# Performance work log

Measured on AMD Instinct MI355X. Metric: run time of the kernel, lower is better.

## Reference

```python
import jax, jax.numpy as jnp
import numpy as np

VOLRADIUS = 256.0
DT = 1.0 / VOLRADIUS  # self.dt = dt / volradius with dt=1.0
N_STEPS = 64
B, H, W, K, M = 1, 256, 256, 64, 16


def setup_inputs() -> dict:
    rng = np.random.default_rng(0)
    # orthographic-ish ray bundle looking down +z through the primitive cloud
    ys, xs = np.meshgrid(np.linspace(-1., 1., H, dtype=np.float32),
                         np.linspace(-1., 1., W, dtype=np.float32), indexing='ij')
    raypos = np.broadcast_to(np.stack([xs, ys, np.full_like(xs, -0.125)], -1)[None],
                             (B, H, W, 3)).astype(np.float32).copy()
    raydir = np.zeros((B, H, W, 3), np.float32); raydir[..., 2] = 1.0
    tmin = np.zeros((B, H, W), np.float32)
    tminmax = np.stack([tmin, tmin + N_STEPS * DT], -1).astype(np.float32)
    # primpos is in WORLD units (module divides by volradius)
    primpos = rng.uniform(-0.1 * VOLRADIUS, 0.1 * VOLRADIUS, (B, K, 3)).astype(np.float32)
    q, _ = np.linalg.qr(rng.normal(size=(B, K, 3, 3)))
    primrot = q.astype(np.float32)
    primscale = rng.uniform(8., 16., (B, K, 3)).astype(np.float32)  # inverse half-extent
    primrgba = rng.uniform(0., 1., (B, K, 4, M, M, M)).astype(np.float32)
    return {
        'raypos': jnp.asarray(raypos), 'raydir': jnp.asarray(raydir),
        'tminmax': jnp.asarray(tminmax), 'primpos': jnp.asarray(primpos),
        'primrot': jnp.asarray(primrot), 'primscale': jnproundtrip(primscale) if False else jnp.asarray(primscale),
        'primrgba': jnp.asarray(primrgba),
    }


def _trilinear_sum(template, pos, primpos, primrot, primscale):
    # template [K,4,M,M,M]; pos [R,3]; returns summed rgba over primitives [R,4]
    Mv = template.shape[-1]
    kidx = jnp.arange(template.shape[0])[None, :]                      # [1,K]
    rel = pos[:, None, :] - primpos[None, :, :]                        # [R,K,3]
    # local = primscale * (primrot^T @ rel), inside prim iff |local| < 1
    local = jnp.einsum('kij,rki->rkj', primrot, rel) * primscale[None]  # [R,K,3]
    inside = jnp.all(jnp.abs(local) < 1.0, axis=-1)                    # [R,K]
    g = jnp.clip((local + 1.0) * 0.5 * (Mv - 1), 0.0, Mv - 1 - 1e-5)    # voxel coords (x,y,z)
    i0 = jnp.clip(jnp.floor(g).astype(jnp.int32), 0, Mv - 2)
    f = g - i0.astype(g.dtype)
    x0, y0, z0 = i0[..., 0], i0[..., 1], i0[..., 2]
    fx, fy, fz = f[..., 0], f[..., 1], f[..., 2]
    c = jnp.zeros(local.shape[:2] + (4,), template.dtype)
    for dz, wz in ((0, 1 - fz), (1, fz)):
        for dy, wy in ((0, 1 - fy), (1, fy)):
            for dx, wx in ((0, 1 - fx), (1, fx)):
                corner = template[kidx, :, z0 + dz, y0 + dy, x0 + dx]  # [R,K,4]
                c = c + corner * (wz * wy * wx)[..., None]
    c = c * inside[..., None]
    return c.sum(axis=1)                                               # [R,4]


def _march(raypos, raydir, tminmax, primpos, primrot, primscale, template):
    Hh, Ww, _ = raypos.shape
    R = Hh * Ww
    o = raypos.reshape(R, 3)
    d = raydir.reshape(R, 3)
    tmm = tminmax.reshape(R, 2)
    tmin, tmax = tmm[:, 0], tmm[:, 1]

    def step(carry, i):
        rgb, alpha = carry
        t = tmin + (i.astype(jnp.float32) + 0.5) * DT
        valid = t < tmax
        pos = o + t[:, None] * d
        s = _trilinear_sum(template, pos, primpos, primrot, primscale)  # [R,4]
        # MVP front-to-back saturating alpha compositing (early-term equivalent)
        contrib = jnp.minimum(1.0, alpha + s[:, 3] * DT) - alpha
        contrib = jnp.where(valid, contrib, 0.0)
        rgb = rgb + s[:, :3] * contrib[:, None]
        alpha = alpha + contrib
        return (rgb, alpha), None

    init = (jnp.zeros((R, 3), jnp.float32), jnp.zeros((R,), jnp.float32))
    (rgb, alpha), _ = jax.lax.scan(jax.checkpoint(step), init, jnp.arange(N_STEPS))
    return jnp.concatenate([rgb, alpha[:, None]], -1).reshape(Hh, Ww, 4)


def reference(raypos, raydir, tminmax, primpos, primrot, primscale, primrgba):
    primpos_n = primpos / VOLRADIUS  # module normalizes primpos by volume radius
    rayrgba = jax.vmap(_march)(raypos, raydir, tminmax, primpos_n, primrot, primscale, primrgba)
    rayrgba = jnp.transpose(rayrgba, (0, 3, 1, 2))  # [B,4,H,W]
    rayrgb = rayrgba[:, :3]
    rayalpha = rayrgba[:, 3:4]
    return rayrgb, rayalpha, rayrgba
```

## Files before the change

kernel.cpp:

```cpp
#include <hip/hip_runtime.h>
#include <hip/hip_fp16.h>

#define Rtot 65536
#define Wimg 256
#define Kp 64
#define NSTEPS 64
#define DTc (1.0f/256.0f)
#define INV_VOLR (1.0f/256.0f)
#define NITEMS 16384
#define HOTGRID 2048

#define PD_OFF    0u
#define TB_OFF    4096u
#define FLAG_OFF  20480u
#define QC_OFF    36864u
#define QUEUE_OFF 40960u
#define LIST_OFF  131072u
#define TT_OFF    2097152u
#define SBUF_OFF  8388608u
#define WS_NEED   (SBUF_OFF + (size_t)NITEMS*256*8)

typedef _Float16 half2v __attribute__((ext_vector_type(2)));

__device__ __forceinline__ half2v u2h(unsigned int u) {
  union { unsigned int u; half2v h; } x; x.u = u; return x.h;
}
__device__ __forceinline__ half2v mkh2(float a, float b) {
  half2v h; h.x = (_Float16)a; h.y = (_Float16)b; return h;
}
__device__ __forceinline__ unsigned int pack2(float a, float b) {
  __half2 h = __floats2half2_rn(a, b);
  return *(unsigned int*)&h;
}

#if __has_builtin(__builtin_amdgcn_fdot2)
#define FDOT2(a, b, c) __builtin_amdgcn_fdot2((a), (b), (c), false)
#else
#define FDOT2(a, b, c) ((float)(a).x*(float)(b).x + (float)(a).y*(float)(b).y + (c))
#endif

__global__ __launch_bounds__(256) void setup_kernel(
    const float* __restrict__ raypos, const float* __restrict__ raydir,
    const float* __restrict__ tminmax, const float* __restrict__ primpos,
    const float* __restrict__ primrot, const float* __restrict__ primscale,
    const float* __restrict__ tmpl,
    float* __restrict__ tb, unsigned long long* __restrict__ tth,
    float* __restrict__ pd, int* __restrict__ qc) {
  int bid = blockIdx.x, tid = threadIdx.x;
  if (bid < 256) {
    __shared__ float smn[4][7], smx[4][7];
    int w = (bid & 15)*16 + (tid & 15);
    int h = (bid >> 4)*16 + (tid >> 4);
    int r = h*Wimg + w;
    float v[7];
    v[0] = raypos[r*3+0]; v[1] = raypos[r*3+1]; v[2] = raypos[r*3+2];
    v[3] = raydir[r*3+0]; v[4] = raydir[r*3+1]; v[5] = raydir[r*3+2];
    v[6] = tminmax[r*2+0];
    float mn[7], mx[7];
#pragma unroll
    for (int i = 0; i < 7; ++i) { mn[i] = v[i]; mx[i] = v[i]; }
#pragma unroll
    for (int m = 1; m < 64; m <<= 1) {
#pragma unroll
      for (int i = 0; i < 7; ++i) {
        mn[i] = fminf(mn[i], __shfl_xor(mn[i], m));
        mx[i] = fmaxf(mx[i], __shfl_xor(mx[i], m));
      }
    }
    int wv = tid >> 6;
    if ((tid & 63) == 0) {
#pragma unroll
      for (int i = 0; i < 7; ++i) { smn[wv][i] = mn[i]; smx[wv][i] = mx[i]; }
    }
    __syncthreads();
    if (tid == 0) {
#pragma unroll
      for (int i = 0; i < 7; ++i) {
        tb[bid*16 + i]     = fminf(fminf(smn[0][i], smn[1][i]), fminf(smn[2][i], smn[3][i]));
        tb[bid*16 + 8 + i] = fmaxf(fmaxf(smx[0][i], smx[1][i]), fmaxf(smx[2][i], smx[3][i]));
      }
    }
  } else if (bid < 512) {
    int k = (bid - 256) >> 2;
    int q = (bid - 256) & 3;
    const float* b0 = tmpl + (((size_t)k) << 14);
    unsigned long long* o = tth + (k << 12);
#pragma unroll
    for (int s = 0; s < 4; ++s) {
      int v = q*1024 + s*256 + tid;
      unsigned long long lo = pack2(b0[v],      b0[4096+v]);
      unsigned long long hi = pack2(b0[8192+v], b0[12288+v]);
      o[v] = lo | (hi << 32);
    }
  } else {
    int k = tid;
    if (k == Kp) qc[0] = 0;
    if (k < Kp) {
      float sc0 = primscale[k*3+0], sc1 = primscale[k*3+1], sc2 = primscale[k*3+2];
      float* o = pd + (k << 4);
      o[0] = primpos[k*3+0] * INV_VOLR;
      o[1] = primpos[k*3+1] * INV_VOLR;
      o[2] = primpos[k*3+2] * INV_VOLR;
      o[3] = 0.0f; o[4] = 0.0f; o[5] = 0.0f;
#pragma unroll
      for (int i = 0; i < 3; ++i) {
        o[6+i*3+0] = primrot[k*9+i*3+0]*sc0;
        o[6+i*3+1] = primrot[k*9+i*3+1]*sc1;
        o[6+i*3+2] = primrot[k*9+i*3+2]*sc2;
      }
      o[15] = 0.0f;
    }
  }
}

__global__ __launch_bounds__(256) void cull_kernel(
    const float* __restrict__ pd, const float* __restrict__ tb,
    unsigned char* __restrict__ flags, unsigned char* __restrict__ lists,
    int* __restrict__ queue, int* __restrict__ qc) {
  int wv = threadIdx.x >> 6, lane = threadIdx.x & 63;
  int item = blockIdx.x*4 + wv;
  int tile = item >> 6, step = item & 63;
  const float* t0 = tb + tile*16;
  float cst = ((float)step + 0.5f)*DTc;
  float tl = t0[6] + cst, th = t0[14] + cst;
  const float* p = pd + (lane << 4);
  float rlo[3], rhi[3];
#pragma unroll
  for (int a = 0; a < 3; ++a) {
    float ol = t0[a], oh = t0[8+a], dl = t0[3+a], dh = t0[11+a];
    float p1 = tl*dl, p2 = tl*dh, p3 = th*dl, p4 = th*dh;
    rlo[a] = ol + fminf(fminf(p1, p2), fminf(p3, p4)) - p[a];
    rhi[a] = oh + fmaxf(fmaxf(p1, p2), fmaxf(p3, p4)) - p[a];
  }
  bool pass = true;
#pragma unroll
  for (int j = 0; j < 3; ++j) {
    float llo = 0.f, lhi = 0.f;
#pragma unroll
    for (int a = 0; a < 3; ++a) {
      float rsc = p[6+a*3+j];
      float q1 = rlo[a]*rsc, q2 = rhi[a]*rsc;
      llo += fminf(q1, q2);
      lhi += fmaxf(q1, q2);
    }
    pass = pass && (llo < 1.0f) && (lhi > -1.0f);
  }
  unsigned long long mask = __ballot(pass);
  int cnt = (int)__popcll(mask);
  if (lane == 0) flags[item] = (unsigned char)(cnt > 0 ? 1 : 0);
  if (pass) {
    int pos = (int)__popcll(mask & ((1ull << lane) - 1ull));
    lists[item*64 + pos] = (unsigned char)lane;
  }
  if (cnt > 0 && lane == 0) {
    int qpos = atomicAdd(qc, 1);
    queue[qpos] = item | (cnt << 16);
  }
}

#define ACC_CORNER(va, vb, wc) {                                             \
    unsigned int alo = (unsigned int)(va), ahi = (unsigned int)((va) >> 32); \
    unsigned int blo = (unsigned int)(vb), bhi = (unsigned int)((vb) >> 32); \
    half2v wp = mkh2((wc)*wx0, (wc)*fx);                                     \
    unsigned int p0 = (alo & 0xFFFFu) | (blo << 16);                         \
    unsigned int p1 = (alo >> 16)     | (bhi ? (blo & 0xFFFF0000u) : (blo & 0xFFFF0000u)); \
    unsigned int p2 = (ahi & 0xFFFFu) | (bhi << 16);                         \
    unsigned int p3 = (ahi >> 16)     | (bhi & 0xFFFF0000u);                 \
    c0 = FDOT2(u2h(p0), wp, c0);                                             \
    c1 = FDOT2(u2h(p1), wp, c1);                                             \
    c2 = FDOT2(u2h(p2), wp, c2);                                             \
    c3 = FDOT2(u2h(p3), wp, c3); }

__global__ __launch_bounds__(256) void shade_kernel(
    const float* __restrict__ raypos, const float* __restrict__ raydir,
    const float* __restrict__ tminmax, const float* __restrict__ pd,
    const unsigned long long* __restrict__ tv,
    const unsigned char* __restrict__ lists,
    const int* __restrict__ queue, const int* __restrict__ qc,
    unsigned long long* __restrict__ sbuf) {
  __shared__ int s_list[Kp];
  int qn = qc[0];
  int tid = threadIdx.x;
  for (int it = blockIdx.x; it < qn; it += HOTGRID) {
    int entry = queue[it];
    int item = entry & 0xFFFF;
    int cnt0 = entry >> 16;
    int tile = item >> 6, step = item & 63;
    __syncthreads();
    if (tid < cnt0) s_list[tid] = lists[item*64 + tid];
    __syncthreads();
    int w = (tile & 15)*16 + (tid & 15);
    int h = (tile >> 4)*16 + (tid >> 4);
    int r = h*Wimg + w;
    float t = tminmax[r*2] + ((float)step + 0.5f)*DTc;
    float px = fmaf(t, raydir[r*3+0], raypos[r*3+0]);
    float py = fmaf(t, raydir[r*3+1], raypos[r*3+1]);
    float pz = fmaf(t, raydir[r*3+2], raypos[r*3+2]);
    float c0 = 0.f, c1 = 0.f, c2 = 0.f, c3 = 0.f;

    for (int j = 0; j < cnt0; ++j) {
      int k = __builtin_amdgcn_readfirstlane(s_list[j]);
      const float* p = pd + (k << 4);
      float relx = px - p[0], rely = py - p[1], relz = pz - p[2];
      float lx = relx*p[6] + rely*p[9]  + relz*p[12];
      float ly = relx*p[7] + rely*p[10] + relz*p[13];
      float lz = relx*p[8] + rely*p[11] + relz*p[14];
      bool inside = fabsf(lx) < 1.0f && fabsf(ly) < 1.0f && fabsf(lz) < 1.0f;
      if (!__any(inside)) continue;
      if (inside) {
        float gx = fminf(fmaxf((lx + 1.0f)*7.5f, 0.0f), 14.99999f);
        float gy = fminf(fmaxf((ly + 1.0f)*7.5f, 0.0f), 14.99999f);
        float gz = fminf(fmaxf((lz + 1.0f)*7.5f, 0.0f), 14.99999f);
        int ix = (int)gx, iy = (int)gy, iz = (int)gz;
        float fx = gx - (float)ix, fy = gy - (float)iy, fz = gz - (float)iz;
        int idx = (k << 12) + iz*256 + iy*16 + ix;
        unsigned long long v00 = tv[idx],       v01 = tv[idx + 1];
        unsigned long long v10 = tv[idx + 16],  v11 = tv[idx + 17];
        unsigned long long v20 = tv[idx + 256], v21 = tv[idx + 257];
        unsigned long long v30 = tv[idx + 272], v31 = tv[idx + 273];
        float wx0 = 1.0f - fx;
        float wy0 = 1.0f - fy, wz0 = 1.0f - fz;
        float w00 = wz0*wy0, w01 = wz0*fy, w10 = fz*wy0, w11 = fz*fy;
        ACC_CORNER(v00, v01, w00)
        ACC_CORNER(v10, v11, w01)
        ACC_CORNER(v20, v21, w10)
        ACC_CORNER(v30, v31, w11)
      }
    }
    unsigned long long pk = ((unsigned long long)pack2(c2, c3) << 32)
                          | (unsigned long long)pack2(c0, c1);
    sbuf[item*256 + tid] = pk;
  }
}

__global__ __launch_bounds__(256) void composite_kernel(
    const float* __restrict__ tminmax, const unsigned long long* __restrict__ sbuf,
    const unsigned char* __restrict__ flags, float* __restrict__ out) {
  __shared__ unsigned char s_flags[NSTEPS];
  int tid = threadIdx.x;
  int b = blockIdx.x;
  if (tid < NSTEPS) s_flags[tid] = flags[b*NSTEPS + tid];
  __syncthreads();
  int w = (b & 15)*16 + (tid & 15);
  int h = (b >> 4)*16 + (tid >> 4);
  int r = h*Wimg + w;
  float tmin = tminmax[r*2+0], tmax = tminmax[r*2+1];
  float rgb0 = 0.f, rgb1 = 0.f, rgb2 = 0.f, alpha = 0.f;
  for (int i = 0; i < NSTEPS; ++i) {
    float s0 = 0.f, s1 = 0.f, s2 = 0.f, s3 = 0.f;
    if (s_flags[i]) {
      unsigned long long pk = sbuf[(b*NSTEPS + i)*256 + tid];
      unsigned int lo = (unsigned int)pk, hi = (unsigned int)(pk >> 32);
      float2 lf = __half22float2(*(__half2*)&lo);
      float2 hf = __half22float2(*(__half2*)&hi);
      s0 = lf.x; s1 = lf.y; s2 = hf.x; s3 = hf.y;
    }
    float t = tmin + ((float)i + 0.5f)*DTc;
    float contrib = fminf(1.0f, fmaf(s3, DTc, alpha)) - alpha;
    contrib = (t < tmax) ? contrib : 0.0f;
    rgb0 = fmaf(s0, contrib, rgb0);
    rgb1 = fmaf(s1, contrib, rgb1);
    rgb2 = fmaf(s2, contrib, rgb2);
    alpha += contrib;
  }
  out[0*Rtot + r] = rgb0;
  out[1*Rtot + r] = rgb1;
  out[2*Rtot + r] = rgb2;
  out[3*Rtot + r] = alpha;
  out[4*Rtot + r] = rgb0;
  out[5*Rtot + r] = rgb1;
  out[6*Rtot + r] = rgb2;
  out[7*Rtot + r] = alpha;
}

__global__ __launch_bounds__(256) void fallback_kernel(
    const float* __restrict__ raypos, const float* __restrict__ raydir,
    const float* __restrict__ tminmax,
    const float* __restrict__ primpos, const float* __restrict__ primrot,
    const float* __restrict__ primscale, const float* __restrict__ tmpl,
    float* __restrict__ out) {
  __shared__ float s_pd[Kp][16];
  int tx = threadIdx.x, ty = threadIdx.y;
  int tid = ty*16 + tx;
  if (tid < Kp) {
    int k = tid;
    float sc0 = primscale[k*3+0], sc1 = primscale[k*3+1], sc2 = primscale[k*3+2];
    s_pd[k][0] = primpos[k*3+0]*INV_VOLR;
    s_pd[k][1] = primpos[k*3+1]*INV_VOLR;
    s_pd[k][2] = primpos[k*3+2]*INV_VOLR;
#pragma unroll
    for (int i = 0; i < 3; ++i) {
      s_pd[k][6+i*3+0] = primrot[k*9+i*3+0]*sc0;
      s_pd[k][6+i*3+1] = primrot[k*9+i*3+1]*sc1;
      s_pd[k][6+i*3+2] = primrot[k*9+i*3+2]*sc2;
    }
  }
  __syncthreads();
  int w = blockIdx.x*16 + tx, h = blockIdx.y*16 + ty;
  int r = h*Wimg + w;
  float ox = raypos[r*3+0], oy = raypos[r*3+1], oz = raypos[r*3+2];
  float dx = raydir[r*3+0], dy = raydir[r*3+1], dz = raydir[r*3+2];
  float tmin = tminmax[r*2+0], tmax = tminmax[r*2+1];
  float rgb0=0.f, rgb1=0.f, rgb2=0.f, alpha=0.f;
  for (int i = 0; i < NSTEPS; ++i) {
    float t = tmin + ((float)i + 0.5f)*DTc;
    float px = fmaf(t, dx, ox), py = fmaf(t, dy, oy), pz = fmaf(t, dz, oz);
    float c[4] = {0.f, 0.f, 0.f, 0.f};
    for (int k = 0; k < Kp; ++k) {
      const float* p = &s_pd[k][0];
      float relx = px - p[0], rely = py - p[1], relz = pz - p[2];
      float lx = relx*p[6] + rely*p[9]  + relz*p[12];
      float ly = relx*p[7] + rely*p[10] + relz*p[13];
      float lz = relx*p[8] + rely*p[11] + relz*p[14];
      if (!(fabsf(lx) < 1.0f && fabsf(ly) < 1.0f && fabsf(lz) < 1.0f)) continue;
      float gx = fminf(fmaxf((lx + 1.0f)*7.5f, 0.0f), 14.99999f);
      float gy = fminf(fmaxf((ly + 1.0f)*7.5f, 0.0f), 14.99999f);
      float gz = fminf(fmaxf((lz + 1.0f)*7.5f, 0.0f), 14.99999f);
      int ix = (int)gx, iy = (int)gy, iz = (int)gz;
      ix = ix > 14 ? 14 : ix; iy = iy > 14 ? 14 : iy; iz = iz > 14 ? 14 : iz;
      float fx = gx - (float)ix, fy = gy - (float)iy, fz = gz - (float)iz;
      float wx0 = 1.0f - fx, wy0 = 1.0f - fy, wz0 = 1.0f - fz;
      float w00 = wz0*wy0, w01 = wz0*fy, w10 = fz*wy0, w11 = fz*fy;
      const float* base = tmpl + (((size_t)k) << 14) + iz*256 + iy*16 + ix;
#pragma unroll
      for (int ch = 0; ch < 4; ++ch) {
        const float* bb = base + ch*4096;
        c[ch] += (bb[0]  *wx0 + bb[1]  *fx) * w00
               + (bb[16] *wx0 + bb[17] *fx) * w01
               + (bb[256]*wx0 + bb[257]*fx) * w10
               + (bb[272]*wx0 + bb[273]*fx) * w11;
      }
    }
    float contrib = fminf(1.0f, fmaf(c[3], DTc, alpha)) - alpha;
    contrib = (t < tmax) ? contrib : 0.0f;
    rgb0 = fmaf(c[0], contrib, rgb0);
    rgb1 = fmaf(c[1], contrib, rgb1);
    rgb2 = fmaf(c[2], contrib, rgb2);
    alpha += contrib;
  }
  out[0*Rtot + r] = rgb0;
  out[1*Rtot + r] = rgb1;
  out[2*Rtot + r] = rgb2;
  out[3*Rtot + r] = alpha;
  out[4*Rtot + r] = rgb0;
  out[5*Rtot + r] = rgb1;
  out[6*Rtot + r] = rgb2;
  out[7*Rtot + r] = alpha;
}

extern "C" void kernel_launch(void* const* d_in, const int* in_sizes, int n_in,
                              void* d_out, int out_size, void* d_ws, size_t ws_size,
                              hipStream_t stream) {
  const float* raypos    = (const float*)d_in[0];
  const float* raydir    = (const float*)d_in[1];
  const float* tminmax   = (const float*)d_in[2];
  const float* primpos   = (const float*)d_in[3];
  const float* primrot   = (const float*)d_in[4];
  const float* primscale = (const float*)d_in[5];
  const float* primrgba  = (const float*)d_in[6];
  float* out = (float*)d_out;

  if (ws_size >= WS_NEED) {
    char* ws = (char*)d_ws;
    float* pd            = (float*)(ws + PD_OFF);
    float* tb            = (float*)(ws + TB_OFF);
    unsigned char* flags = (unsigned char*)(ws + FLAG_OFF);
    int* qc              = (int*)(ws + QC_OFF);
    int* queue           = (int*)(ws + QUEUE_OFF);
    unsigned char* lists = (unsigned char*)(ws + LIST_OFF);
    unsigned long long* tth  = (unsigned long long*)(ws + TT_OFF);
    unsigned long long* sbuf = (unsigned long long*)(ws + SBUF_OFF);

    setup_kernel<<<513, 256, 0, stream>>>(raypos, raydir, tminmax, primpos,
                                          primrot, primscale, primrgba,
                                          tb, tth, pd, qc);
    cull_kernel<<<NITEMS/4, 256, 0, stream>>>(pd, tb, flags, lists, queue, qc);
    shade_kernel<<<HOTGRID, 256, 0, stream>>>(raypos, raydir, tminmax, pd,
                                              tth, lists, queue, qc, sbuf);
    composite_kernel<<<256, 256, 0, stream>>>(tminmax, sbuf, flags, out);
  } else {
    fallback_kernel<<<dim3(16,16), dim3(16,16), 0, stream>>>(
        raypos, raydir, tminmax, primpos, primrot, primscale, primrgba, out);
  }
}
```

Before: 84.10 us.

## Fuse culling into shade kernel and store x-neighbor pairs in 16-byte texels

Removes the separate cull kernel, global queue, atomic counter and per-item lists; each shade block now culls its own tile-step in the first wavefront and builds the primitive list in shared memory, exiting early when empty. The template is re-packed so each 16-byte texel holds both x-neighbours for all four channels, so the 8 gathers per sample become 4 wider loads with no bit-shuffling. This trades one kernel launch and queue traffic for a grid of 16384 blocks, many of which exit immediately, and doubles the size of the packed template.

```diff
diff --git a/kernel.cpp b/kernel.cpp
--- a/kernel.cpp
+++ b/kernel.cpp
@@ -8,15 +8,11 @@
 #define DTc (1.0f/256.0f)
 #define INV_VOLR (1.0f/256.0f)
 #define NITEMS 16384
-#define HOTGRID 2048
 
 #define PD_OFF    0u
 #define TB_OFF    4096u
 #define FLAG_OFF  20480u
-#define QC_OFF    36864u
-#define QUEUE_OFF 40960u
-#define LIST_OFF  131072u
-#define TT_OFF    2097152u
+#define TT_OFF    65536u
 #define SBUF_OFF  8388608u
 #define WS_NEED   (SBUF_OFF + (size_t)NITEMS*256*8)
 
@@ -44,8 +40,7 @@
     const float* __restrict__ tminmax, const float* __restrict__ primpos,
     const float* __restrict__ primrot, const float* __restrict__ primscale,
     const float* __restrict__ tmpl,
-    float* __restrict__ tb, unsigned long long* __restrict__ tth,
-    float* __restrict__ pd, int* __restrict__ qc) {
+    float* __restrict__ tb, uint4* __restrict__ tth, float* __restrict__ pd) {
   int bid = blockIdx.x, tid = threadIdx.x;
   if (bid < 256) {
     __shared__ float smn[4][7], smx[4][7];
@@ -84,17 +79,21 @@
     int k = (bid - 256) >> 2;
     int q = (bid - 256) & 3;
     const float* b0 = tmpl + (((size_t)k) << 14);
-    unsigned long long* o = tth + (k << 12);
+    uint4* o = tth + (k << 12);
 #pragma unroll
     for (int s = 0; s < 4; ++s) {
       int v = q*1024 + s*256 + tid;
-      unsigned long long lo = pack2(b0[v],      b0[4096+v]);
-      unsigned long long hi = pack2(b0[8192+v], b0[12288+v]);
-      o[v] = lo | (hi << 32);
+      int x = v & 15;
+      int xn = (x < 15) ? v + 1 : v;
+      uint4 qq;
+      qq.x = pack2(b0[v],       b0[xn]);
+      qq.y = pack2(b0[4096+v],  b0[4096+xn]);
+      qq.z = pack2(b0[8192+v],  b0[8192+xn]);
+      qq.w = pack2(b0[12288+v], b0[12288+xn]);
+      o[v] = qq;
     }
   } else {
     int k = tid;
-    if (k == Kp) qc[0] = 0;
     if (k < Kp) {
       float sc0 = primscale[k*3+0], sc1 = primscale[k*3+1], sc2 = primscale[k*3+2];
       float* o = pd + (k << 4);
@@ -113,124 +112,108 @@
   }
 }
 
-__global__ __launch_bounds__(256) void cull_kernel(
-    const float* __restrict__ pd, const float* __restrict__ tb,
-    unsigned char* __restrict__ flags, unsigned char* __restrict__ lists,
-    int* __restrict__ queue, int* __restrict__ qc) {
-  int wv = threadIdx.x >> 6, lane = threadIdx.x & 63;
-  int item = blockIdx.x*4 + wv;
-  int tile = item >> 6, step = item & 63;
-  const float* t0 = tb + tile*16;
-  float cst = ((float)step + 0.5f)*DTc;
-  float tl = t0[6] + cst, th = t0[14] + cst;
-  const float* p = pd + (lane << 4);
-  float rlo[3], rhi[3];
-#pragma unroll
-  for (int a = 0; a < 3; ++a) {
-    float ol = t0[a], oh = t0[8+a], dl = t0[3+a], dh = t0[11+a];
-    float p1 = tl*dl, p2 = tl*dh, p3 = th*dl, p4 = th*dh;
-    rlo[a] = ol + fminf(fminf(p1, p2), fminf(p3, p4)) - p[a];
-    rhi[a] = oh + fmaxf(fmaxf(p1, p2), fmaxf(p3, p4)) - p[a];
-  }
-  bool pass = true;
-#pragma unroll
-  for (int j = 0; j < 3; ++j) {
-    float llo = 0.f, lhi = 0.f;
-#pragma unroll
-    for (int a = 0; a < 3; ++a) {
-      float rsc = p[6+a*3+j];
-      float q1 = rlo[a]*rsc, q2 = rhi[a]*rsc;
-      llo += fminf(q1, q2);
-      lhi += fmaxf(q1, q2);
-    }
-    pass = pass && (llo < 1.0f) && (lhi > -1.0f);
-  }
-  unsigned long long mask = __ballot(pass);
-  int cnt = (int)__popcll(mask);
-  if (lane == 0) flags[item] = (unsigned char)(cnt > 0 ? 1 : 0);
-  if (pass) {
-    int pos = (int)__popcll(mask & ((1ull << lane) - 1ull));
-    lists[item*64 + pos] = (unsigned char)lane;
-  }
-  if (cnt > 0 && lane == 0) {
-    int qpos = atomicAdd(qc, 1);
-    queue[qpos] = item | (cnt << 16);
-  }
-}
-
-#define ACC_CORNER(va, vb, wc) {                                             \
-    unsigned int alo = (unsigned int)(va), ahi = (unsigned int)((va) >> 32); \
-    unsigned int blo = (unsigned int)(vb), bhi = (unsigned int)((vb) >> 32); \
-    half2v wp = mkh2((wc)*wx0, (wc)*fx);                                     \
-    unsigned int p0 = (alo & 0xFFFFu) | (blo << 16);                         \
-    unsigned int p1 = (alo >> 16)     | (bhi ? (blo & 0xFFFF0000u) : (blo & 0xFFFF0000u)); \
-    unsigned int p2 = (ahi & 0xFFFFu) | (bhi << 16);                         \
-    unsigned int p3 = (ahi >> 16)     | (bhi & 0xFFFF0000u);                 \
-    c0 = FDOT2(u2h(p0), wp, c0);                                             \
-    c1 = FDOT2(u2h(p1), wp, c1);                                             \
-    c2 = FDOT2(u2h(p2), wp, c2);                                             \
-    c3 = FDOT2(u2h(p3), wp, c3); }
-
 __global__ __launch_bounds__(256) void shade_kernel(
     const float* __restrict__ raypos, const float* __restrict__ raydir,
     const float* __restrict__ tminmax, const float* __restrict__ pd,
-    const unsigned long long* __restrict__ tv,
-    const unsigned char* __restrict__ lists,
-    const int* __restrict__ queue, const int* __restrict__ qc,
-    unsigned long long* __restrict__ sbuf) {
+    const float* __restrict__ tb, const uint4* __restrict__ tth,
+    unsigned long long* __restrict__ sbuf, unsigned char* __restrict__ flags) {
   __shared__ int s_list[Kp];
-  int qn = qc[0];
+  __shared__ int s_cnt;
+  int item = blockIdx.x;
+  int tile = item >> 6, step = item & 63;
   int tid = threadIdx.x;
-  for (int it = blockIdx.x; it < qn; it += HOTGRID) {
-    int entry = queue[it];
-    int item = entry & 0xFFFF;
-    int cnt0 = entry >> 16;
-    int tile = item >> 6, step = item & 63;
-    __syncthreads();
-    if (tid < cnt0) s_list[tid] = lists[item*64 + tid];
-    __syncthreads();
-    int w = (tile & 15)*16 + (tid & 15);
-    int h = (tile >> 4)*16 + (tid >> 4);
-    int r = h*Wimg + w;
-    float t = tminmax[r*2] + ((float)step + 0.5f)*DTc;
-    float px = fmaf(t, raydir[r*3+0], raypos[r*3+0]);
-    float py = fmaf(t, raydir[r*3+1], raypos[r*3+1]);
-    float pz = fmaf(t, raydir[r*3+2], raypos[r*3+2]);
-    float c0 = 0.f, c1 = 0.f, c2 = 0.f, c3 = 0.f;
-
-    for (int j = 0; j < cnt0; ++j) {
-      int k = __builtin_amdgcn_readfirstlane(s_list[j]);
-      const float* p = pd + (k << 4);
-      float relx = px - p[0], rely = py - p[1], relz = pz - p[2];
-      float lx = relx*p[6] + rely*p[9]  + relz*p[12];
-      float ly = relx*p[7] + rely*p[10] + relz*p[13];
-      float lz = relx*p[8] + rely*p[11] + relz*p[14];
-      bool inside = fabsf(lx) < 1.0f && fabsf(ly) < 1.0f && fabsf(lz) < 1.0f;
-      if (!__any(inside)) continue;
-      if (inside) {
-        float gx = fminf(fmaxf((lx + 1.0f)*7.5f, 0.0f), 14.99999f);
-        float gy = fminf(fmaxf((ly + 1.0f)*7.5f, 0.0f), 14.99999f);
-        float gz = fminf(fmaxf((lz + 1.0f)*7.5f, 0.0f), 14.99999f);
-        int ix = (int)gx, iy = (int)gy, iz = (int)gz;
-        float fx = gx - (float)ix, fy = gy - (float)iy, fz = gz - (float)iz;
-        int idx = (k << 12) + iz*256 + iy*16 + ix;
-        unsigned long long v00 = tv[idx],       v01 = tv[idx + 1];
-        unsigned long long v10 = tv[idx + 16],  v11 = tv[idx + 17];
-        unsigned long long v20 = tv[idx + 256], v21 = tv[idx + 257];
-        unsigned long long v30 = tv[idx + 272], v31 = tv[idx + 273];
-        float wx0 = 1.0f - fx;
-        float wy0 = 1.0f - fy, wz0 = 1.0f - fz;
-        float w00 = wz0*wy0, w01 = wz0*fy, w10 = fz*wy0, w11 = fz*fy;
-        ACC_CORNER(v00, v01, w00)
-        ACC_CORNER(v10, v11, w01)
-        ACC_CORNER(v20, v21, w10)
-        ACC_CORNER(v30, v31, w11)
-      }
-    }
-    unsigned long long pk = ((unsigned long long)pack2(c2, c3) << 32)
-                          | (unsigned long long)pack2(c0, c1);
-    sbuf[item*256 + tid] = pk;
-  }
+  if (tid < 64) {
+    const float* t0 = tb + tile*16;
+    float cst = ((float)step + 0.5f)*DTc;
+    float tl = t0[6] + cst, th = t0[14] + cst;
+    const float* p = pd + (tid << 4);
+    float rlo[3], rhi[3];
+#pragma unroll
+    for (int a = 0; a < 3; ++a) {
+      float ol = t0[a], oh = t0[8+a], dl = t0[3+a], dh = t0[11+a];
+      float p1 = tl*dl, p2 = tl*dh, p3 = th*dl, p4 = th*dh;
+      rlo[a] = ol + fminf(fminf(p1, p2), fminf(p3, p4)) - p[a];
+      rhi[a] = oh + fmaxf(fmaxf(p1, p2), fmaxf(p3, p4)) - p[a];
+    }
+    bool pass = true;
+#pragma unroll
+    for (int j = 0; j < 3; ++j) {
+      float llo = 0.f, lhi = 0.f;
+#pragma unroll
+      for (int a = 0; a < 3; ++a) {
+        float rsc = p[6+a*3+j];
+        float q1 = rlo[a]*rsc, q2 = rhi[a]*rsc;
+        llo += fminf(q1, q2);
+        lhi += fmaxf(q1, q2);
+      }
+      pass = pass && (llo < 1.0f) && (lhi > -1.0f);
+    }
+    unsigned long long mask = __ballot(pass);
+    if (tid == 0) s_cnt = (int)__popcll(mask);
+    if (pass) {
+      int pos = (int)__popcll(mask & ((1ull << tid) - 1ull));
+      s_list[pos] = tid;
+    }
+  }
+  __syncthreads();
+  int cnt = s_cnt;
+  if (tid == 0) flags[item] = (unsigned char)(cnt > 0 ? 1 : 0);
+  if (cnt == 0) return;
+
+  int w = (tile & 15)*16 + (tid & 15);
+  int h = (tile >> 4)*16 + (tid >> 4);
+  int r = h*Wimg + w;
+  float t = tminmax[r*2] + ((float)step + 0.5f)*DTc;
+  float px = fmaf(t, raydir[r*3+0], raypos[r*3+0]);
+  float py = fmaf(t, raydir[r*3+1], raypos[r*3+1]);
+  float pz = fmaf(t, raydir[r*3+2], raypos[r*3+2]);
+  float c0 = 0.f, c1 = 0.f, c2 = 0.f, c3 = 0.f;
+
+  for (int j = 0; j < cnt; ++j) {
+    int k = __builtin_amdgcn_readfirstlane(s_list[j]);
+    const float* p = pd + (k << 4);
+    float relx = px - p[0], rely = py - p[1], relz = pz - p[2];
+    float lx = relx*p[6] + rely*p[9]  + relz*p[12];
+    float ly = relx*p[7] + rely*p[10] + relz*p[13];
+    float lz = relx*p[8] + rely*p[11] + relz*p[14];
+    bool inside = fabsf(lx) < 1.0f && fabsf(ly) < 1.0f && fabsf(lz) < 1.0f;
+    if (!__any(inside)) continue;
+    if (inside) {
+      float gx = fminf(fmaxf((lx + 1.0f)*7.5f, 0.0f), 14.99999f);
+      float gy = fminf(fmaxf((ly + 1.0f)*7.5f, 0.0f), 14.99999f);
+      float gz = fminf(fmaxf((lz + 1.0f)*7.5f, 0.0f), 14.99999f);
+      int ix = (int)gx, iy = (int)gy, iz = (int)gz;
+      float fx = gx - (float)ix, fy = gy - (float)iy, fz = gz - (float)iz;
+      float wx0 = 1.0f - fx;
+      float wy0 = 1.0f - fy, wz0 = 1.0f - fz;
+      float w00 = wz0*wy0, w01 = wz0*fy, w10 = fz*wy0, w11 = fz*fy;
+      const uint4* a = tth + ((size_t)k << 12) + (iz*256 + iy*16 + ix);
+      uint4 q0 = a[0], q1 = a[16], q2 = a[256], q3 = a[272];
+      half2v wp0 = mkh2(w00*wx0, w00*fx);
+      half2v wp1 = mkh2(w01*wx0, w01*fx);
+      half2v wp2 = mkh2(w10*wx0, w10*fx);
+      half2v wp3 = mkh2(w11*wx0, w11*fx);
+      c0 = FDOT2(u2h(q0.x), wp0, c0);
+      c1 = FDOT2(u2h(q0.y), wp0, c1);
+      c2 = FDOT2(u2h(q0.z), wp0, c2);
+      c3 = FDOT2(u2h(q0.w), wp0, c3);
+      c0 = FDOT2(u2h(q1.x), wp1, c0);
+      c1 = FDOT2(u2h(q1.y), wp1, c1);
+      c2 = FDOT2(u2h(q1.z), wp1, c2);
+      c3 = FDOT2(u2h(q1.w), wp1, c3);
+      c0 = FDOT2(u2h(q2.x), wp2, c0);
+      c1 = FDOT2(u2h(q2.y), wp2, c1);
+      c2 = FDOT2(u2h(q2.z), wp2, c2);
+      c3 = FDOT2(u2h(q2.w), wp2, c3);
+      c0 = FDOT2(u2h(q3.x), wp3, c0);
+      c1 = FDOT2(u2h(q3.y), wp3, c1);
+      c2 = FDOT2(u2h(q3.z), wp3, c2);
+      c3 = FDOT2(u2h(q3.w), wp3, c3);
+    }
+  }
+  unsigned long long pk = ((unsigned long long)pack2(c2, c3) << 32)
+                        | (unsigned long long)pack2(c0, c1);
+  sbuf[item*256 + tid] = pk;
 }
 
 __global__ __launch_bounds__(256) void composite_kernel(
@@ -365,18 +348,14 @@
     float* pd            = (float*)(ws + PD_OFF);
     float* tb            = (float*)(ws + TB_OFF);
     unsigned char* flags = (unsigned char*)(ws + FLAG_OFF);
-    int* qc              = (int*)(ws + QC_OFF);
-    int* queue           = (int*)(ws + QUEUE_OFF);
-    unsigned char* lists = (unsigned char*)(ws + LIST_OFF);
-    unsigned long long* tth  = (unsigned long long*)(ws + TT_OFF);
+    uint4* tth           = (uint4*)(ws + TT_OFF);
     unsigned long long* sbuf = (unsigned long long*)(ws + SBUF_OFF);
 
     setup_kernel<<<513, 256, 0, stream>>>(raypos, raydir, tminmax, primpos,
                                           primrot, primscale, primrgba,
-                                          tb, tth, pd, qc);
-    cull_kernel<<<NITEMS/4, 256, 0, stream>>>(pd, tb, flags, lists, queue, qc);
-    shade_kernel<<<HOTGRID, 256, 0, stream>>>(raypos, raydir, tminmax, pd,
-                                              tth, lists, queue, qc, sbuf);
+                                          tb, tth, pd);
+    shade_kernel<<<NITEMS, 256, 0, stream>>>(raypos, raydir, tminmax, pd, tb,
+                                             tth, sbuf, flags);
     composite_kernel<<<256, 256, 0, stream>>>(tminmax, sbuf, flags, out);
   } else {
     fallback_kernel<<<dim3(16,16), dim3(16,16), 0, stream>>>(
```

Result: faster. 67.60 us, median of 2 (-19.6%).
